# Kernel optimization log

Measured on AMD Instinct MI355X. Metric: run time of the kernel, lower is better.

The kernel has to match this reference:

```python
import jax, jax.numpy as jnp
import numpy as np

B, F, H, E, V, T = 128, 2048, 1024, 512, 16384, 20
TEMP = 1.0


def setup_inputs() -> dict:
    key = jax.random.key(0)
    ks = jax.random.split(key, 12)
    sc = lambda i, shape, s=0.02: jax.random.normal(ks[i], shape, jnp.float32) * s
    # Gumbel(0,1) noise for RelaxedOneHotCategorical.rsample
    u = jax.random.uniform(ks[11], (T, B, V), jnp.float32, 1e-6, 1.0 - 1e-6)
    gumbel = -jnp.log(-jnp.log(u))
    return dict(
        image_features=jax.random.normal(ks[0], (B, F), jnp.float32),
        agent_w=sc(1, (H, F)),
        agent_b=jnp.zeros((H,), jnp.float32),
        w_ih=sc(2, (3 * H, E)),
        w_hh=sc(3, (3 * H, H)),
        b_ih=jnp.zeros((3 * H,), jnp.float32),
        b_hh=jnp.zeros((3 * H,), jnp.float32),
        w_out=sc(4, (V, H)),
        b_out=jnp.zeros((V,), jnp.float32),
        emb_w=sc(5, (E, V)),
        sos=sc(6, (E,), 0.01),
        gumbel=gumbel,
    )


def _gru_cell(x, h, w_ih, w_hh, b_ih, b_hh):
    # torch.nn.GRUCell math
    gi = x @ w_ih.T + b_ih          # [B, 3H]
    gh = h @ w_hh.T + b_hh          # [B, 3H]
    i_r, i_z, i_n = jnp.split(gi, 3, axis=-1)
    h_r, h_z, h_n = jnp.split(gh, 3, axis=-1)
    r = jax.nn.sigmoid(i_r + h_r)
    z = jax.nn.sigmoid(i_z + h_z)
    n = jnp.tanh(i_n + r * h_n)
    return (1.0 - z) * n + z * h


def reference(image_features, agent_w, agent_b, w_ih, w_hh, b_ih, b_hh,
              w_out, b_out, emb_w, sos, gumbel):
    h0 = image_features @ agent_w.T + agent_b                 # agent: [B, H]
    e0 = jnp.broadcast_to(sos, (image_features.shape[0], sos.shape[0]))  # SOS embed

    def step(carry, g_t):
        h, e = carry
        h = _gru_cell(e, h, w_ih, w_hh, b_ih, b_hh)            # [B, H]
        logits = h @ w_out.T + b_out                           # [B, V]
        # Gumbel-softmax sample (training mode, not straight-through)
        x = jax.nn.softmax((logits + g_t) / TEMP, axis=-1)     # [B, V]
        e = x @ emb_w.T                                        # soft-one-hot embedding, [B, E]
        return (h, e), x

    _, seq = jax.lax.scan(step, (h0, e0), gumbel)              # [T, B, V]
    return jnp.transpose(seq, (1, 0, 2))                       # [B, T, V]
```

## Files before the change

kernel.cpp:

```cpp
#include <hip/hip_runtime.h>
#include <hip/hip_bf16.h>
#include <math.h>

namespace {

constexpr int kB = 128, kF = 2048, kH = 1024, kE = 512, kV = 16384, kT = 20;

typedef __attribute__((ext_vector_type(4))) float f32x4;
typedef __attribute__((ext_vector_type(8))) short bf16x8;

#define MFMA(a, b, c) __builtin_amdgcn_mfma_f32_16x16x32_bf16((a), (b), (c), 0, 0, 0)

__device__ __forceinline__ short f2bf(float f) {
  union { float f; unsigned u; } un;
  un.f = f;
  unsigned x = un.u;
  x += 0x7fffu + ((x >> 16) & 1u);
  return (short)(x >> 16);
}

__device__ __forceinline__ float bf2f(short s) {
  union { unsigned u; float f; } un;
  un.u = ((unsigned)(unsigned short)s) << 16;
  return un.f;
}

__device__ __forceinline__ float sigm(float x) { return 1.0f / (1.0f + __expf(-x)); }

__device__ __forceinline__ void cvt4(const float* __restrict__ s, short* __restrict__ d,
                                     long n4, long gid, long gs) {
  for (long i = gid; i < n4; i += gs) {
    float4 v = ((const float4*)s)[i];
    short4 o;
    o.x = f2bf(v.x); o.y = f2bf(v.y); o.z = f2bf(v.z); o.w = f2bf(v.w);
    ((short4*)d)[i] = o;
  }
}

__global__ __launch_bounds__(256) void k_convert(
    const float* __restrict__ wout, const float* __restrict__ emb,
    const float* __restrict__ wih, const float* __restrict__ whh,
    const float* __restrict__ aw, const float* __restrict__ img,
    const float* __restrict__ sos,
    short* __restrict__ wout_b, short* __restrict__ emb_b,
    short* __restrict__ wih_b, short* __restrict__ whh_b,
    short* __restrict__ aw_b, short* __restrict__ img_b,
    float* __restrict__ e_f) {
  long gid = (long)blockIdx.x * blockDim.x + threadIdx.x;
  long gs = (long)gridDim.x * blockDim.x;
  cvt4(wout, wout_b, (long)kV * kH / 4, gid, gs);
  cvt4(emb, emb_b, (long)kE * kV / 4, gid, gs);
  cvt4(wih, wih_b, (long)3 * kH * kE / 4, gid, gs);
  cvt4(whh, whh_b, (long)3 * kH * kH / 4, gid, gs);
  cvt4(aw, aw_b, (long)kH * kF / 4, gid, gs);
  cvt4(img, img_b, (long)kB * kF / 4, gid, gs);
  for (long i = gid; i < kB * kE; i += gs) e_f[i] = sos[i & (kE - 1)];
}

__global__ __launch_bounds__(256) void k_h0(const short* __restrict__ img_b,
                                            const short* __restrict__ aw_b,
                                            const float* __restrict__ ab,
                                            float* __restrict__ hf, short* __restrict__ hb) {
  int tid = threadIdx.x;
  int l = tid & 63, w = tid >> 6;
  int lr = l & 15, g = l >> 4, lk = g * 8;
  int col0 = blockIdx.x * 16;
  int row0 = w * 32;
  f32x4 acc[2] = {};
#pragma unroll 4
  for (int k0 = 0; k0 < kF; k0 += 32) {
    bf16x8 a0 = *(const bf16x8*)&img_b[(row0 + lr) * kF + k0 + lk];
    bf16x8 a1 = *(const bf16x8*)&img_b[(row0 + 16 + lr) * kF + k0 + lk];
    bf16x8 b = *(const bf16x8*)&aw_b[(size_t)(col0 + lr) * kF + k0 + lk];
    acc[0] = MFMA(a0, b, acc[0]);
    acc[1] = MFMA(a1, b, acc[1]);
  }
  int col = col0 + lr;
  float bias = ab[col];
#pragma unroll
  for (int mf = 0; mf < 2; ++mf)
#pragma unroll
    for (int j = 0; j < 4; ++j) {
      int row = row0 + mf * 16 + g * 4 + j;
      float v = acc[mf][j] + bias;
      hf[row * kH + col] = v;
      hb[row * kH + col] = f2bf(v);
    }
}

__global__ __launch_bounds__(512) void k_gru(
    const float* __restrict__ e_f, const short* __restrict__ hb_prev,
    float* __restrict__ hf,
    const short* __restrict__ wih_b, const short* __restrict__ whh_b,
    const float* __restrict__ bih, const float* __restrict__ bhh,
    short* __restrict__ hb_next, float* __restrict__ denom_cur,
    const short* __restrict__ p_prev, const float* __restrict__ denom_prev,
    float* __restrict__ out_prev) {
  int tid = threadIdx.x, bid = blockIdx.x;
  int l = tid & 63, w = tid >> 6;
  int lr = l & 15, g = l >> 4, lk = g * 8;
  __shared__ f32x4 part[4][2][2][64];
  int colt = bid >> 2, rq = bid & 3;
  int col0 = colt * 16;
  if (w < 4) {
    int rh = w & 1, kq = w >> 1;
    int row0 = rq * 32 + rh * 16;
    if (bid == 0 && tid < 32) {
      f32x4 z = {0.0f, 0.0f, 0.0f, 0.0f};
      *(f32x4*)&denom_cur[tid * 4] = z;
    }
    f32x4 ar = {}, az = {}, ain = {}, ahn = {};
    if (kq == 0) {
#pragma unroll 4
      for (int ki = 0; ki < 16; ++ki) {
        int k0 = ki * 32;
        float4 af0 = *(const float4*)&e_f[(row0 + lr) * kE + k0 + lk];
        float4 af1 = *(const float4*)&e_f[(row0 + lr) * kE + k0 + lk + 4];
        bf16x8 a;
        a[0] = f2bf(af0.x); a[1] = f2bf(af0.y); a[2] = f2bf(af0.z); a[3] = f2bf(af0.w);
        a[4] = f2bf(af1.x); a[5] = f2bf(af1.y); a[6] = f2bf(af1.z); a[7] = f2bf(af1.w);
        bf16x8 br = *(const bf16x8*)&wih_b[(size_t)(col0 + lr) * kE + k0 + lk];
        bf16x8 bz = *(const bf16x8*)&wih_b[(size_t)(kH + col0 + lr) * kE + k0 + lk];
        bf16x8 bn = *(const bf16x8*)&wih_b[(size_t)(2 * kH + col0 + lr) * kE + k0 + lk];
        ar = MFMA(a, br, ar);
        az = MFMA(a, bz, az);
        ain = MFMA(a, bn, ain);
      }
#pragma unroll 4
      for (int ki = 0; ki < 8; ++ki) {
        int k0 = ki * 32;
        bf16x8 a = *(const bf16x8*)&hb_prev[(row0 + lr) * kH + k0 + lk];
        bf16x8 br = *(const bf16x8*)&whh_b[(size_t)(col0 + lr) * kH + k0 + lk];
        bf16x8 bz = *(const bf16x8*)&whh_b[(size_t)(kH + col0 + lr) * kH + k0 + lk];
        bf16x8 bn = *(const bf16x8*)&whh_b[(size_t)(2 * kH + col0 + lr) * kH + k0 + lk];
        ar = MFMA(a, br, ar);
        az = MFMA(a, bz, az);
        ahn = MFMA(a, bn, ahn);
      }
    } else {
#pragma unroll 4
      for (int ki = 0; ki < 24; ++ki) {
        int k0 = 256 + ki * 32;
        bf16x8 a = *(const bf16x8*)&hb_prev[(row0 + lr) * kH + k0 + lk];
        bf16x8 br = *(const bf16x8*)&whh_b[(size_t)(col0 + lr) * kH + k0 + lk];
        bf16x8 bz = *(const bf16x8*)&whh_b[(size_t)(kH + col0 + lr) * kH + k0 + lk];
        bf16x8 bn = *(const bf16x8*)&whh_b[(size_t)(2 * kH + col0 + lr) * kH + k0 + lk];
        ar = MFMA(a, br, ar);
        az = MFMA(a, bz, az);
        ahn = MFMA(a, bn, ahn);
      }
    }
    part[0][rh][kq][l] = ar;
    part[1][rh][kq][l] = az;
    part[2][rh][kq][l] = ain;
    part[3][rh][kq][l] = ahn;
  } else if (out_prev != nullptr) {
    int r = bid >> 1, halfc = bid & 1;
    float rd = 1.0f / denom_prev[r];
    int coff = halfc * 8192 + (w - 4) * 2048 + l * 32;
    const short* pr = p_prev + (size_t)r * kV + coff;
    float* orow = out_prev + (size_t)r * (kT * kV) + coff;
#pragma unroll
    for (int jj = 0; jj < 4; ++jj) {
      bf16x8 p8 = *(const bf16x8*)(pr + jj * 8);
      f32x4 o0, o1;
      o0[0] = bf2f(p8[0]) * rd; o0[1] = bf2f(p8[1]) * rd;
      o0[2] = bf2f(p8[2]) * rd; o0[3] = bf2f(p8[3]) * rd;
      o1[0] = bf2f(p8[4]) * rd; o1[1] = bf2f(p8[5]) * rd;
      o1[2] = bf2f(p8[6]) * rd; o1[3] = bf2f(p8[7]) * rd;
      __builtin_nontemporal_store(o0, (f32x4*)(orow + jj * 8));
      __builtin_nontemporal_store(o1, (f32x4*)(orow + jj * 8 + 4));
    }
  }
  __syncthreads();
  if (w < 2) {
    int rh2 = w;
    int row0e = rq * 32 + rh2 * 16;
    f32x4 rs = part[0][rh2][0][l] + part[0][rh2][1][l];
    f32x4 zs = part[1][rh2][0][l] + part[1][rh2][1][l];
    f32x4 is = part[2][rh2][0][l] + part[2][rh2][1][l];
    f32x4 hs = part[3][rh2][0][l] + part[3][rh2][1][l];
    int col = col0 + lr;
    float bihr = bih[col], bhhr = bhh[col];
    float bihz = bih[kH + col], bhhz = bhh[kH + col];
    float bihn = bih[2 * kH + col], bhhn = bhh[2 * kH + col];
#pragma unroll
    for (int j = 0; j < 4; ++j) {
      int row = row0e + g * 4 + j;
      float r = sigm(rs[j] + bihr + bhhr);
      float z = sigm(zs[j] + bihz + bhhz);
      float nn = tanhf(is[j] + bihn + r * (hs[j] + bhhn));
      float hv = (1.0f - z) * nn + z * hf[row * kH + col];
      hf[row * kH + col] = hv;
      hb_next[row * kH + col] = f2bf(hv);
    }
  }
}

__global__ __launch_bounds__(512) void k_logits(
    const short* __restrict__ h_b, const short* __restrict__ wout_b,
    const float* __restrict__ bout, const float* __restrict__ gum_t,
    short* __restrict__ p_b, float* __restrict__ denom, float* __restrict__ e_f) {
  int tid = threadIdx.x;
  int l = tid & 63, w = tid >> 6;
  int lr = l & 15, g = l >> 4, lk = g * 8;
  int wm = w >> 2, wn = w & 3;
  int n0 = blockIdx.x * 64;
  int col = n0 + wn * 16 + lr;
  int row0 = wm * 64;
  int gi = blockIdx.x * 512 + tid;
  if (gi < kB * kE) e_f[gi] = 0.0f;
  float gmr[16];
#pragma unroll
  for (int mf = 0; mf < 4; ++mf)
#pragma unroll
    for (int j = 0; j < 4; ++j)
      gmr[mf * 4 + j] = __builtin_nontemporal_load(
          &gum_t[(size_t)(row0 + mf * 16 + g * 4 + j) * kV + col]);
  float bo = bout[col];
  const short* Bp = &wout_b[(size_t)col * kH + lk];
  f32x4 acc[4] = {};
  bf16x8 brg[8], arg[2][4];
#pragma unroll
  for (int k = 0; k < 8; ++k) brg[k] = *(const bf16x8*)(Bp + k * 32);
#pragma unroll
  for (int k = 0; k < 2; ++k)
#pragma unroll
    for (int mf = 0; mf < 4; ++mf)
      arg[k][mf] = *(const bf16x8*)&h_b[(row0 + mf * 16 + lr) * kH + k * 32 + lk];
#pragma unroll
  for (int k = 0; k < 32; ++k) {
    acc[0] = MFMA(arg[k & 1][0], brg[k & 7], acc[0]);
    acc[1] = MFMA(arg[k & 1][1], brg[k & 7], acc[1]);
    acc[2] = MFMA(arg[k & 1][2], brg[k & 7], acc[2]);
    acc[3] = MFMA(arg[k & 1][3], brg[k & 7], acc[3]);
    if (k < 24) brg[k & 7] = *(const bf16x8*)(Bp + (k + 8) * 32);
    if (k < 30) {
#pragma unroll
      for (int mf = 0; mf < 4; ++mf)
        arg[k & 1][mf] =
            *(const bf16x8*)&h_b[(row0 + mf * 16 + lr) * kH + (k + 2) * 32 + lk];
    }
  }
  __shared__ float ls[2][4][64];
  float p[16];
#pragma unroll
  for (int i = 0; i < 16; ++i) p[i] = __expf(acc[i >> 2][i & 3] + bo + gmr[i]);
#pragma unroll
  for (int i = 0; i < 16; ++i) {
    int rl = (i >> 2) * 16 + g * 4 + (i & 3);
    p_b[(size_t)(row0 + rl) * kV + col] = f2bf(p[i]);
  }
#pragma unroll
  for (int i = 0; i < 16; ++i) {
    float s = p[i];
#pragma unroll
    for (int sf = 1; sf < 16; sf <<= 1) s += __shfl_xor(s, sf, 64);
    if (lr == 0) ls[wm][wn][(i >> 2) * 16 + g * 4 + (i & 3)] = s;
  }
  __syncthreads();
  if (tid < 128) {
    int row = tid, wmm = tid >> 6, rl = tid & 63;
    float sb = ls[wmm][0][rl] + ls[wmm][1][rl] + ls[wmm][2][rl] + ls[wmm][3][rl];
    atomicAdd(&denom[row], sb);
  }
}

__global__ __launch_bounds__(512) void k_e(
    const short* __restrict__ p_b, const float* __restrict__ denom,
    const short* __restrict__ emb_b, float* __restrict__ e_f) {
  int tid = threadIdx.x;
  int l = tid & 63, w = tid >> 6;
  int lr = l & 15, g = l >> 4, lk = g * 8;
  int wm = w >> 2, wn = w & 3;
  int kc = blockIdx.x >> 3, et = blockIdx.x & 7;
  int kbase = kc * 512;
  int colB = et * 64 + wn * 16 + lr;
  __shared__ float s_rd[kB];
  if (tid < kB) s_rd[tid] = 1.0f / denom[tid];
  __shared__ bf16x8 xs8[2048];
  char* xs = (char*)xs8;
  int colg = tid & 15, rrow = tid >> 4;
  f32x4 acc[4] = {};
  __syncthreads();
  for (int s = 0; s < 4; ++s) {
    if (s) __syncthreads();
#pragma unroll
    for (int rr = 0; rr < 4; ++rr) {
      int row = rr * 32 + rrow;
      int cb = s * 128 + colg * 8;
      bf16x8 p8 = *(const bf16x8*)&p_b[(size_t)row * kV + kbase + cb];
      float scl = s_rd[row];
      bf16x8 xv;
#pragma unroll
      for (int i = 0; i < 8; ++i) xv[i] = f2bf(bf2f(p8[i]) * scl);
      unsigned off = (unsigned)(row * 256 + colg * 16) ^ ((row & 7) << 4);
      *(bf16x8*)(xs + off) = xv;
    }
    __syncthreads();
#pragma unroll
    for (int kk = 0; kk < 4; ++kk) {
      bf16x8 b = *(const bf16x8*)&emb_b[(size_t)colB * kV + kbase + s * 128 + kk * 32 + lk];
#pragma unroll
      for (int mf = 0; mf < 4; ++mf) {
        int rowa = wm * 64 + mf * 16 + lr;
        unsigned off = (unsigned)(rowa * 256 + (kk * 32 + lk) * 2) ^ ((rowa & 7) << 4);
        bf16x8 a = *(const bf16x8*)(xs + off);
        acc[mf] = MFMA(a, b, acc[mf]);
      }
    }
  }
#pragma unroll
  for (int mf = 0; mf < 4; ++mf)
#pragma unroll
    for (int j = 0; j < 4; ++j) {
      int row = wm * 64 + mf * 16 + g * 4 + j;
      atomicAdd(&e_f[row * kE + et * 64 + wn * 16 + lr], acc[mf][j]);
    }
}

__global__ __launch_bounds__(256) void k_out(const short* __restrict__ p_b,
                                             const float* __restrict__ denom,
                                             float* __restrict__ outp) {
  int tid = threadIdx.x, bid = blockIdx.x;
  int r = bid >> 1, halfc = bid & 1;
  float rd = 1.0f / denom[r];
  int coff = halfc * 8192 + tid * 32;
  const short* pr = p_b + (size_t)r * kV + coff;
  float* orow = outp + (size_t)r * (kT * kV) + coff;
#pragma unroll
  for (int jj = 0; jj < 4; ++jj) {
    bf16x8 p8 = *(const bf16x8*)(pr + jj * 8);
    f32x4 o0, o1;
    o0[0] = bf2f(p8[0]) * rd; o0[1] = bf2f(p8[1]) * rd;
    o0[2] = bf2f(p8[2]) * rd; o0[3] = bf2f(p8[3]) * rd;
    o1[0] = bf2f(p8[4]) * rd; o1[1] = bf2f(p8[5]) * rd;
    o1[2] = bf2f(p8[6]) * rd; o1[3] = bf2f(p8[7]) * rd;
    __builtin_nontemporal_store(o0, (f32x4*)(orow + jj * 8));
    __builtin_nontemporal_store(o1, (f32x4*)(orow + jj * 8 + 4));
  }
}

}

extern "C" void kernel_launch(void* const* d_in, const int* in_sizes, int n_in,
                              void* d_out, int out_size, void* d_ws, size_t ws_size,
                              hipStream_t stream) {
  const float* img = (const float*)d_in[0];
  const float* aw = (const float*)d_in[1];
  const float* ab = (const float*)d_in[2];
  const float* wih = (const float*)d_in[3];
  const float* whh = (const float*)d_in[4];
  const float* bih = (const float*)d_in[5];
  const float* bhh = (const float*)d_in[6];
  const float* wout = (const float*)d_in[7];
  const float* bout = (const float*)d_in[8];
  const float* emb = (const float*)d_in[9];
  const float* sos = (const float*)d_in[10];
  const float* gum = (const float*)d_in[11];
  float* out = (float*)d_out;
  char* ws = (char*)d_ws;

  short* wout_b = (short*)(ws + 0);
  short* emb_b = (short*)(ws + 33554432);
  short* wih_b = (short*)(ws + 50331648);
  short* whh_b = (short*)(ws + 53477376);
  short* aw_b = (short*)(ws + 59768832);
  short* img_b = (short*)(ws + 63963136);
  float* hf = (float*)(ws + 64487424);
  short* hb0 = (short*)(ws + 65011712);
  short* hb1 = (short*)(ws + 65273856);
  short* p_b = (short*)(ws + 65536000);
  float* denoms = (float*)(ws + 69730304);
  float* e_f = (float*)(ws + 69732352);

  short* hb[2] = {hb0, hb1};

  k_convert<<<2048, 256, 0, stream>>>(wout, emb, wih, whh, aw, img, sos, wout_b, emb_b,
                                      wih_b, whh_b, aw_b, img_b, e_f);
  k_h0<<<64, 256, 0, stream>>>(img_b, aw_b, ab, hf, hb[0]);
  for (int t = 0; t < kT; ++t) {
    int rp = t & 1, wp = rp ^ 1;
    float* denomC = denoms + (t & 1) * 256;
    float* denomP = denoms + ((t & 1) ^ 1) * 256;
    float* out_prev = (t == 0) ? nullptr : out + (size_t)(t - 1) * kV;
    k_gru<<<256, 512, 0, stream>>>(e_f, hb[rp], hf, wih_b, whh_b, bih, bhh, hb[wp],
                                   denomC, p_b, denomP, out_prev);
    k_logits<<<256, 512, 0, stream>>>(hb[wp], wout_b, bout, gum + (size_t)t * kB * kV,
                                      p_b, denomC, e_f);
    k_e<<<256, 512, 0, stream>>>(p_b, denomC, emb_b, e_f);
  }
  k_out<<<256, 256, 0, stream>>>(p_b, denoms + 256, out + (size_t)(kT - 1) * kV);
}
```

Baseline: 1.896 ms.

## Double grid sizes of GRU, logits and embedding kernels to fill more CUs

The per-step kernels are re-partitioned so each launches 512 blocks instead of 256. The GRU kernel now uses 256-thread blocks over 16-row tiles with a four-way K split, and each thread does half of the output write-back. The logits kernel uses 32-column tiles, and the embedding kernel uses a 256-wide K chunk. The goal is to occupy all compute units on a 256-CU part and cut per-step latency, at the cost of more atomic adds, more partial-sum traffic and less operand reuse per block.

New measurement: 1.944 ms. 2.5% more time.

```diff
diff --git a/kernel.cpp b/kernel.cpp
--- a/kernel.cpp
+++ b/kernel.cpp
@@ -88,7 +88,7 @@
     }
 }
 
-__global__ __launch_bounds__(512) void k_gru(
+__global__ __launch_bounds__(256) void k_gru(
     const float* __restrict__ e_f, const short* __restrict__ hb_prev,
     float* __restrict__ hf,
     const short* __restrict__ wih_b, const short* __restrict__ whh_b,
@@ -99,69 +99,15 @@
   int tid = threadIdx.x, bid = blockIdx.x;
   int l = tid & 63, w = tid >> 6;
   int lr = l & 15, g = l >> 4, lk = g * 8;
-  __shared__ f32x4 part[4][2][2][64];
-  int colt = bid >> 2, rq = bid & 3;
-  int col0 = colt * 16;
-  if (w < 4) {
-    int rh = w & 1, kq = w >> 1;
-    int row0 = rq * 32 + rh * 16;
-    if (bid == 0 && tid < 32) {
-      f32x4 z = {0.0f, 0.0f, 0.0f, 0.0f};
-      *(f32x4*)&denom_cur[tid * 4] = z;
-    }
-    f32x4 ar = {}, az = {}, ain = {}, ahn = {};
-    if (kq == 0) {
-#pragma unroll 4
-      for (int ki = 0; ki < 16; ++ki) {
-        int k0 = ki * 32;
-        float4 af0 = *(const float4*)&e_f[(row0 + lr) * kE + k0 + lk];
-        float4 af1 = *(const float4*)&e_f[(row0 + lr) * kE + k0 + lk + 4];
-        bf16x8 a;
-        a[0] = f2bf(af0.x); a[1] = f2bf(af0.y); a[2] = f2bf(af0.z); a[3] = f2bf(af0.w);
-        a[4] = f2bf(af1.x); a[5] = f2bf(af1.y); a[6] = f2bf(af1.z); a[7] = f2bf(af1.w);
-        bf16x8 br = *(const bf16x8*)&wih_b[(size_t)(col0 + lr) * kE + k0 + lk];
-        bf16x8 bz = *(const bf16x8*)&wih_b[(size_t)(kH + col0 + lr) * kE + k0 + lk];
-        bf16x8 bn = *(const bf16x8*)&wih_b[(size_t)(2 * kH + col0 + lr) * kE + k0 + lk];
-        ar = MFMA(a, br, ar);
-        az = MFMA(a, bz, az);
-        ain = MFMA(a, bn, ain);
-      }
-#pragma unroll 4
-      for (int ki = 0; ki < 8; ++ki) {
-        int k0 = ki * 32;
-        bf16x8 a = *(const bf16x8*)&hb_prev[(row0 + lr) * kH + k0 + lk];
-        bf16x8 br = *(const bf16x8*)&whh_b[(size_t)(col0 + lr) * kH + k0 + lk];
-        bf16x8 bz = *(const bf16x8*)&whh_b[(size_t)(kH + col0 + lr) * kH + k0 + lk];
-        bf16x8 bn = *(const bf16x8*)&whh_b[(size_t)(2 * kH + col0 + lr) * kH + k0 + lk];
-        ar = MFMA(a, br, ar);
-        az = MFMA(a, bz, az);
-        ahn = MFMA(a, bn, ahn);
-      }
-    } else {
-#pragma unroll 4
-      for (int ki = 0; ki < 24; ++ki) {
-        int k0 = 256 + ki * 32;
-        bf16x8 a = *(const bf16x8*)&hb_prev[(row0 + lr) * kH + k0 + lk];
-        bf16x8 br = *(const bf16x8*)&whh_b[(size_t)(col0 + lr) * kH + k0 + lk];
-        bf16x8 bz = *(const bf16x8*)&whh_b[(size_t)(kH + col0 + lr) * kH + k0 + lk];
-        bf16x8 bn = *(const bf16x8*)&whh_b[(size_t)(2 * kH + col0 + lr) * kH + k0 + lk];
-        ar = MFMA(a, br, ar);
-        az = MFMA(a, bz, az);
-        ahn = MFMA(a, bn, ahn);
-      }
-    }
-    part[0][rh][kq][l] = ar;
-    part[1][rh][kq][l] = az;
-    part[2][rh][kq][l] = ain;
-    part[3][rh][kq][l] = ahn;
-  } else if (out_prev != nullptr) {
-    int r = bid >> 1, halfc = bid & 1;
+  __shared__ f32x4 part[4][4][64];
+  if (out_prev != nullptr) {
+    int r = bid >> 2, q = bid & 3;
     float rd = 1.0f / denom_prev[r];
-    int coff = halfc * 8192 + (w - 4) * 2048 + l * 32;
+    int coff = q * 4096 + tid * 16;
     const short* pr = p_prev + (size_t)r * kV + coff;
     float* orow = out_prev + (size_t)r * (kT * kV) + coff;
 #pragma unroll
-    for (int jj = 0; jj < 4; ++jj) {
+    for (int jj = 0; jj < 2; ++jj) {
       bf16x8 p8 = *(const bf16x8*)(pr + jj * 8);
       f32x4 o0, o1;
       o0[0] = bf2f(p8[0]) * rd; o0[1] = bf2f(p8[1]) * rd;
@@ -172,21 +118,57 @@
       __builtin_nontemporal_store(o1, (f32x4*)(orow + jj * 8 + 4));
     }
   }
+  if (bid == 0 && tid < 32) {
+    f32x4 z = {0.0f, 0.0f, 0.0f, 0.0f};
+    *(f32x4*)&denom_cur[tid * 4] = z;
+  }
+  int colt = bid & 63, rq = bid >> 6;
+  int col0 = colt * 16, row0 = rq * 16;
+  int kq = w;
+  f32x4 ar = {}, az = {}, ain = {}, ahn = {};
+#pragma unroll
+  for (int ki = 0; ki < 4; ++ki) {
+    int k0 = kq * 128 + ki * 32;
+    float4 af0 = *(const float4*)&e_f[(row0 + lr) * kE + k0 + lk];
+    float4 af1 = *(const float4*)&e_f[(row0 + lr) * kE + k0 + lk + 4];
+    bf16x8 a;
+    a[0] = f2bf(af0.x); a[1] = f2bf(af0.y); a[2] = f2bf(af0.z); a[3] = f2bf(af0.w);
+    a[4] = f2bf(af1.x); a[5] = f2bf(af1.y); a[6] = f2bf(af1.z); a[7] = f2bf(af1.w);
+    bf16x8 br = *(const bf16x8*)&wih_b[(size_t)(col0 + lr) * kE + k0 + lk];
+    bf16x8 bz = *(const bf16x8*)&wih_b[(size_t)(kH + col0 + lr) * kE + k0 + lk];
+    bf16x8 bn = *(const bf16x8*)&wih_b[(size_t)(2 * kH + col0 + lr) * kE + k0 + lk];
+    ar = MFMA(a, br, ar);
+    az = MFMA(a, bz, az);
+    ain = MFMA(a, bn, ain);
+  }
+#pragma unroll
+  for (int ki = 0; ki < 8; ++ki) {
+    int k0 = kq * 256 + ki * 32;
+    bf16x8 a = *(const bf16x8*)&hb_prev[(row0 + lr) * kH + k0 + lk];
+    bf16x8 br = *(const bf16x8*)&whh_b[(size_t)(col0 + lr) * kH + k0 + lk];
+    bf16x8 bz = *(const bf16x8*)&whh_b[(size_t)(kH + col0 + lr) * kH + k0 + lk];
+    bf16x8 bn = *(const bf16x8*)&whh_b[(size_t)(2 * kH + col0 + lr) * kH + k0 + lk];
+    ar = MFMA(a, br, ar);
+    az = MFMA(a, bz, az);
+    ahn = MFMA(a, bn, ahn);
+  }
+  part[0][kq][l] = ar;
+  part[1][kq][l] = az;
+  part[2][kq][l] = ain;
+  part[3][kq][l] = ahn;
   __syncthreads();
-  if (w < 2) {
-    int rh2 = w;
-    int row0e = rq * 32 + rh2 * 16;
-    f32x4 rs = part[0][rh2][0][l] + part[0][rh2][1][l];
-    f32x4 zs = part[1][rh2][0][l] + part[1][rh2][1][l];
-    f32x4 is = part[2][rh2][0][l] + part[2][rh2][1][l];
-    f32x4 hs = part[3][rh2][0][l] + part[3][rh2][1][l];
+  if (w == 0) {
+    f32x4 rs = part[0][0][l] + part[0][1][l] + part[0][2][l] + part[0][3][l];
+    f32x4 zs = part[1][0][l] + part[1][1][l] + part[1][2][l] + part[1][3][l];
+    f32x4 is = part[2][0][l] + part[2][1][l] + part[2][2][l] + part[2][3][l];
+    f32x4 hs = part[3][0][l] + part[3][1][l] + part[3][2][l] + part[3][3][l];
     int col = col0 + lr;
     float bihr = bih[col], bhhr = bhh[col];
     float bihz = bih[kH + col], bhhz = bhh[kH + col];
     float bihn = bih[2 * kH + col], bhhn = bhh[2 * kH + col];
 #pragma unroll
     for (int j = 0; j < 4; ++j) {
-      int row = row0e + g * 4 + j;
+      int row = row0 + g * 4 + j;
       float r = sigm(rs[j] + bihr + bhhr);
       float z = sigm(zs[j] + bihz + bhhz);
       float nn = tanhf(is[j] + bihn + r * (hs[j] + bhhn));
@@ -197,62 +179,59 @@
   }
 }
 
-__global__ __launch_bounds__(512) void k_logits(
+__global__ __launch_bounds__(512, 4) void k_logits(
     const short* __restrict__ h_b, const short* __restrict__ wout_b,
     const float* __restrict__ bout, const float* __restrict__ gum_t,
     short* __restrict__ p_b, float* __restrict__ denom, float* __restrict__ e_f) {
   int tid = threadIdx.x;
   int l = tid & 63, w = tid >> 6;
   int lr = l & 15, g = l >> 4, lk = g * 8;
-  int wm = w >> 2, wn = w & 3;
-  int n0 = blockIdx.x * 64;
-  int col = n0 + wn * 16 + lr;
-  int row0 = wm * 64;
+  int wm = w >> 1, wn = w & 1;
+  int col = blockIdx.x * 32 + wn * 16 + lr;
+  int row0 = wm * 32;
   int gi = blockIdx.x * 512 + tid;
   if (gi < kB * kE) e_f[gi] = 0.0f;
-  float gmr[16];
-#pragma unroll
-  for (int mf = 0; mf < 4; ++mf)
+  float gmr[8];
+#pragma unroll
+  for (int mf = 0; mf < 2; ++mf)
 #pragma unroll
     for (int j = 0; j < 4; ++j)
       gmr[mf * 4 + j] = __builtin_nontemporal_load(
           &gum_t[(size_t)(row0 + mf * 16 + g * 4 + j) * kV + col]);
   float bo = bout[col];
   const short* Bp = &wout_b[(size_t)col * kH + lk];
-  f32x4 acc[4] = {};
-  bf16x8 brg[8], arg[2][4];
+  f32x4 acc[2] = {};
+  bf16x8 brg[8], arg[2][2];
 #pragma unroll
   for (int k = 0; k < 8; ++k) brg[k] = *(const bf16x8*)(Bp + k * 32);
 #pragma unroll
   for (int k = 0; k < 2; ++k)
 #pragma unroll
-    for (int mf = 0; mf < 4; ++mf)
+    for (int mf = 0; mf < 2; ++mf)
       arg[k][mf] = *(const bf16x8*)&h_b[(row0 + mf * 16 + lr) * kH + k * 32 + lk];
 #pragma unroll
   for (int k = 0; k < 32; ++k) {
     acc[0] = MFMA(arg[k & 1][0], brg[k & 7], acc[0]);
     acc[1] = MFMA(arg[k & 1][1], brg[k & 7], acc[1]);
-    acc[2] = MFMA(arg[k & 1][2], brg[k & 7], acc[2]);
-    acc[3] = MFMA(arg[k & 1][3], brg[k & 7], acc[3]);
     if (k < 24) brg[k & 7] = *(const bf16x8*)(Bp + (k + 8) * 32);
     if (k < 30) {
 #pragma unroll
-      for (int mf = 0; mf < 4; ++mf)
+      for (int mf = 0; mf < 2; ++mf)
         arg[k & 1][mf] =
             *(const bf16x8*)&h_b[(row0 + mf * 16 + lr) * kH + (k + 2) * 32 + lk];
     }
   }
-  __shared__ float ls[2][4][64];
-  float p[16];
-#pragma unroll
-  for (int i = 0; i < 16; ++i) p[i] = __expf(acc[i >> 2][i & 3] + bo + gmr[i]);
-#pragma unroll
-  for (int i = 0; i < 16; ++i) {
+  __shared__ float ls[4][2][32];
+  float p[8];
+#pragma unroll
+  for (int i = 0; i < 8; ++i) p[i] = __expf(acc[i >> 2][i & 3] + bo + gmr[i]);
+#pragma unroll
+  for (int i = 0; i < 8; ++i) {
     int rl = (i >> 2) * 16 + g * 4 + (i & 3);
     p_b[(size_t)(row0 + rl) * kV + col] = f2bf(p[i]);
   }
 #pragma unroll
-  for (int i = 0; i < 16; ++i) {
+  for (int i = 0; i < 8; ++i) {
     float s = p[i];
 #pragma unroll
     for (int sf = 1; sf < 16; sf <<= 1) s += __shfl_xor(s, sf, 64);
@@ -260,13 +239,13 @@
   }
   __syncthreads();
   if (tid < 128) {
-    int row = tid, wmm = tid >> 6, rl = tid & 63;
-    float sb = ls[wmm][0][rl] + ls[wmm][1][rl] + ls[wmm][2][rl] + ls[wmm][3][rl];
+    int row = tid;
+    float sb = ls[row >> 5][0][row & 31] + ls[row >> 5][1][row & 31];
     atomicAdd(&denom[row], sb);
   }
 }
 
-__global__ __launch_bounds__(512) void k_e(
+__global__ __launch_bounds__(512, 4) void k_e(
     const short* __restrict__ p_b, const float* __restrict__ denom,
     const short* __restrict__ emb_b, float* __restrict__ e_f) {
   int tid = threadIdx.x;
@@ -274,7 +253,7 @@
   int lr = l & 15, g = l >> 4, lk = g * 8;
   int wm = w >> 2, wn = w & 3;
   int kc = blockIdx.x >> 3, et = blockIdx.x & 7;
-  int kbase = kc * 512;
+  int kbase = kc * 256;
   int colB = et * 64 + wn * 16 + lr;
   __shared__ float s_rd[kB];
   if (tid < kB) s_rd[tid] = 1.0f / denom[tid];
@@ -283,7 +262,7 @@
   int colg = tid & 15, rrow = tid >> 4;
   f32x4 acc[4] = {};
   __syncthreads();
-  for (int s = 0; s < 4; ++s) {
+  for (int s = 0; s < 2; ++s) {
     if (s) __syncthreads();
 #pragma unroll
     for (int rr = 0; rr < 4; ++rr) {
@@ -384,11 +363,11 @@
     float* denomC = denoms + (t & 1) * 256;
     float* denomP = denoms + ((t & 1) ^ 1) * 256;
     float* out_prev = (t == 0) ? nullptr : out + (size_t)(t - 1) * kV;
-    k_gru<<<256, 512, 0, stream>>>(e_f, hb[rp], hf, wih_b, whh_b, bih, bhh, hb[wp],
+    k_gru<<<512, 256, 0, stream>>>(e_f, hb[rp], hf, wih_b, whh_b, bih, bhh, hb[wp],
                                    denomC, p_b, denomP, out_prev);
-    k_logits<<<256, 512, 0, stream>>>(hb[wp], wout_b, bout, gum + (size_t)t * kB * kV,
+    k_logits<<<512, 512, 0, stream>>>(hb[wp], wout_b, bout, gum + (size_t)t * kB * kV,
                                       p_b, denomC, e_f);
-    k_e<<<256, 512, 0, stream>>>(p_b, denomC, emb_b, e_f);
+    k_e<<<512, 512, 0, stream>>>(p_b, denomC, emb_b, e_f);
   }
   k_out<<<256, 256, 0, stream>>>(p_b, denoms + 256, out + (size_t)(kT - 1) * kV);
 }
```

## Stage W_out tiles in LDS and shrink logits blocks to 32 columns

Applied to the files above, without the earlier changes.

The logits kernel now copies each block's 32-row slice of the bf16 output weight into padded shared memory. Both row-group waves read their B fragments from that copy instead of each loading them from global memory. The grid doubles to 512 blocks of 256 threads, with launch bounds asking for two resident blocks per CU, to improve occupancy and spread the work across more blocks. In exchange, the whole weight slice must load before a barrier, so the earlier register prefetch pipeline that overlapped B loads with MFMAs is gone, and each block uses about 66KB of LDS.

Result: slower. 1.935 ms (+2.0%).

```diff
diff --git a/kernel.cpp b/kernel.cpp
--- a/kernel.cpp
+++ b/kernel.cpp
@@ -197,18 +197,19 @@
   }
 }
 
-__global__ __launch_bounds__(512) void k_logits(
+__global__ __launch_bounds__(256, 2) void k_logits(
     const short* __restrict__ h_b, const short* __restrict__ wout_b,
     const float* __restrict__ bout, const float* __restrict__ gum_t,
     short* __restrict__ p_b, float* __restrict__ denom, float* __restrict__ e_f) {
+  __shared__ char lds[32 * 2064];
+  __shared__ float ls[2][2][64];
   int tid = threadIdx.x;
   int l = tid & 63, w = tid >> 6;
   int lr = l & 15, g = l >> 4, lk = g * 8;
-  int wm = w >> 2, wn = w & 3;
-  int n0 = blockIdx.x * 64;
-  int col = n0 + wn * 16 + lr;
-  int row0 = wm * 64;
-  int gi = blockIdx.x * 512 + tid;
+  int wm = w & 1, wn = w >> 1;
+  int col = blockIdx.x * 32 + wn * 16 + lr;
+  int mrow0 = wm * 64;
+  int gi = blockIdx.x * 256 + tid;
   if (gi < kB * kE) e_f[gi] = 0.0f;
   float gmr[16];
 #pragma unroll
@@ -216,40 +217,49 @@
 #pragma unroll
     for (int j = 0; j < 4; ++j)
       gmr[mf * 4 + j] = __builtin_nontemporal_load(
-          &gum_t[(size_t)(row0 + mf * 16 + g * 4 + j) * kV + col]);
+          &gum_t[(size_t)(mrow0 + mf * 16 + g * 4 + j) * kV + col]);
   float bo = bout[col];
-  const short* Bp = &wout_b[(size_t)col * kH + lk];
+  {
+    const char* src = (const char*)(wout_b + (size_t)blockIdx.x * 32 * kH);
+#pragma unroll
+    for (int i = 0; i < 16; ++i) {
+      int c = tid + i * 256;
+      int row = c >> 7;
+      int within = (c & 127) * 16;
+      bf16x8 v = *(const bf16x8*)(src + c * 16);
+      *(bf16x8*)(&lds[row * 2064 + within]) = v;
+    }
+  }
+  __syncthreads();
+  const char* bbase = &lds[(wn * 16 + lr) * 2064 + lk * 2];
   f32x4 acc[4] = {};
-  bf16x8 brg[8], arg[2][4];
-#pragma unroll
-  for (int k = 0; k < 8; ++k) brg[k] = *(const bf16x8*)(Bp + k * 32);
+  bf16x8 arg[2][4];
 #pragma unroll
   for (int k = 0; k < 2; ++k)
 #pragma unroll
     for (int mf = 0; mf < 4; ++mf)
-      arg[k][mf] = *(const bf16x8*)&h_b[(row0 + mf * 16 + lr) * kH + k * 32 + lk];
+      arg[k][mf] = *(const bf16x8*)&h_b[(mrow0 + mf * 16 + lr) * kH + k * 32 + lk];
 #pragma unroll
   for (int k = 0; k < 32; ++k) {
-    acc[0] = MFMA(arg[k & 1][0], brg[k & 7], acc[0]);
-    acc[1] = MFMA(arg[k & 1][1], brg[k & 7], acc[1]);
-    acc[2] = MFMA(arg[k & 1][2], brg[k & 7], acc[2]);
-    acc[3] = MFMA(arg[k & 1][3], brg[k & 7], acc[3]);
-    if (k < 24) brg[k & 7] = *(const bf16x8*)(Bp + (k + 8) * 32);
+    bf16x8 b = *(const bf16x8*)(bbase + k * 64);
+    acc[0] = MFMA(arg[k & 1][0], b, acc[0]);
+    acc[1] = MFMA(arg[k & 1][1], b, acc[1]);
+    acc[2] = MFMA(arg[k & 1][2], b, acc[2]);
+    acc[3] = MFMA(arg[k & 1][3], b, acc[3]);
     if (k < 30) {
 #pragma unroll
       for (int mf = 0; mf < 4; ++mf)
         arg[k & 1][mf] =
-            *(const bf16x8*)&h_b[(row0 + mf * 16 + lr) * kH + (k + 2) * 32 + lk];
-    }
-  }
-  __shared__ float ls[2][4][64];
+            *(const bf16x8*)&h_b[(mrow0 + mf * 16 + lr) * kH + (k + 2) * 32 + lk];
+    }
+  }
   float p[16];
 #pragma unroll
   for (int i = 0; i < 16; ++i) p[i] = __expf(acc[i >> 2][i & 3] + bo + gmr[i]);
 #pragma unroll
   for (int i = 0; i < 16; ++i) {
     int rl = (i >> 2) * 16 + g * 4 + (i & 3);
-    p_b[(size_t)(row0 + rl) * kV + col] = f2bf(p[i]);
+    p_b[(size_t)(mrow0 + rl) * kV + col] = f2bf(p[i]);
   }
 #pragma unroll
   for (int i = 0; i < 16; ++i) {
@@ -260,8 +270,8 @@
   }
   __syncthreads();
   if (tid < 128) {
-    int row = tid, wmm = tid >> 6, rl = tid & 63;
-    float sb = ls[wmm][0][rl] + ls[wmm][1][rl] + ls[wmm][2][rl] + ls[wmm][3][rl];
+    int row = tid;
+    float sb = ls[row >> 6][0][row & 63] + ls[row >> 6][1][row & 63];
     atomicAdd(&denom[row], sb);
   }
 }
@@ -386,7 +396,7 @@
     float* out_prev = (t == 0) ? nullptr : out + (size_t)(t - 1) * kV;
     k_gru<<<256, 512, 0, stream>>>(e_f, hb[rp], hf, wih_b, whh_b, bih, bhh, hb[wp],
                                    denomC, p_b, denomP, out_prev);
-    k_logits<<<256, 512, 0, stream>>>(hb[wp], wout_b, bout, gum + (size_t)t * kB * kV,
+    k_logits<<<512, 256, 0, stream>>>(hb[wp], wout_b, bout, gum + (size_t)t * kB * kV,
                                       p_b, denomC, e_f);
     k_e<<<256, 512, 0, stream>>>(p_b, denomC, emb_b, e_f);
   }
```
